# Optimization experiments

Hardware: AMD Instinct MI355X
Metric: run time of the kernel (lower is better)

The kernel has to match this reference:

```python
import jax, jax.numpy as jnp
import numpy as np

B, S, IN, IN2, H = 512, 256, 300, 300, 512
FN = 3  # filter_num


def setup_inputs() -> dict:
    key = jax.random.key(0)
    ks = jax.random.split(key, 16)
    def n(k, shape, scale=0.05):
        return jax.random.normal(k, shape, dtype=jnp.float32) * scale
    return {
        "x": jax.random.normal(ks[0], (B, S, IN), dtype=jnp.float32),
        "W_in": n(ks[1], (IN, IN2)), "b_in": n(ks[2], (IN2,)),
        "Wih": n(ks[3], (IN2, 4 * H)), "Whh": n(ks[4], (H, 4 * H)),
        "bih": n(ks[5], (4 * H,)), "bhh": n(ks[6], (4 * H,)),
        "Q": n(ks[7], (H, IN2)), "R": n(ks[8], (IN2, H)),
        "Wc3": n(ks[9], (FN, 1, 3, H)), "bc3": n(ks[10], (FN,)),
        "Wc4": n(ks[11], (FN, 1, 4, H)), "bc4": n(ks[12], (FN,)),
        "Wc5": n(ks[13], (FN, 1, 5, H)), "bc5": n(ks[14], (FN,)),
        "W_lin": n(ks[15], (3 * FN, 2)), "b_lin": jnp.zeros((2,), jnp.float32),
    }


def reference(x, W_in, b_in, Wih, Whh, bih, bhh, Q, R,
              Wc3, bc3, Wc4, bc4, Wc5, bc5, W_lin, b_lin):
    # input projection: [B,S,IN] -> [B,S,IN2]
    xin = jnp.tanh(x @ W_in + b_in)
    xs = jnp.swapaxes(xin, 0, 1)  # [S,B,IN2] for scan
    bsz = x.shape[0]
    h0 = jnp.zeros((bsz, H), x.dtype)
    c0 = jnp.zeros((bsz, H), x.dtype)

    def step(carry, xt):
        ht, Ct = carry
        # mogrify, mog_iterations=2: i=1 odd updates x, i=2 even updates h
        xt = 2.0 * jax.nn.sigmoid(ht @ Q) * xt
        ht = 2.0 * jax.nn.sigmoid(xt @ R) * ht
        gates = xt @ Wih + bih + ht @ Whh + bhh  # [B,4H]
        i, f, g, o = jnp.split(gates, 4, axis=1)
        Ct = jax.nn.sigmoid(f) * Ct + jax.nn.sigmoid(i) * jnp.tanh(g)
        ht = jax.nn.sigmoid(o) * jnp.tanh(Ct)
        return (ht, Ct), ht

    _, hs = jax.lax.scan(step, (h0, c0), xs)  # [S,B,H]
    hmap = jnp.swapaxes(hs, 0, 1)[:, None, :, :]  # [B,1,S,H]

    feats = []
    for w, b in ((Wc3, bc3), (Wc4, bc4), (Wc5, bc5)):
        y = jax.lax.conv_general_dilated(
            hmap, w, (1, 1), 'VALID',
            dimension_numbers=('NCHW', 'OIHW', 'NCHW'))
        y = jax.nn.relu(y + b[None, :, None, None])  # [B,FN,S-fsz+1,1]
        feats.append(jnp.max(y, axis=(2, 3)))  # global max pool -> [B,FN]
    cat = jnp.concatenate(feats, axis=1)  # [B, 3*FN]
    # dropout is identity at inference
    return cat @ W_lin + b_lin  # [B,2]
```

## Files before the change

### kernel.cpp

```cpp
#include <hip/hip_runtime.h>

#define DI __device__ __forceinline__

typedef __attribute__((ext_vector_type(4))) float  f32x4;
typedef __attribute__((ext_vector_type(8))) short  s16x8;
typedef __attribute__((ext_vector_type(8))) __bf16 bf16x8;
typedef unsigned long long u64;

constexpr int S_   = 256;
constexpr int B_   = 512;
constexpr int H_   = 512;
constexpr int KP_  = 320;
constexpr int ALD_ = 832;
constexpr int NRING = 34;
constexpr int NWG  = 256;
constexpr size_t HSLOT = 512 * 512;

constexpr size_t OFF_XIN = 0;
constexpr size_t SZ_XIN  = (size_t)S_ * B_ * KP_ * 2;
constexpr size_t OFF_U   = OFF_XIN + SZ_XIN;
constexpr size_t SZ_U    = (size_t)B_ * S_ * 64 * 4;
constexpr size_t OFF_HS  = OFF_U + SZ_U;
constexpr size_t SZ_HS   = (size_t)NRING * HSLOT * 2;
constexpr size_t OFF_ACT = OFF_HS + SZ_HS;
constexpr size_t SZ_ACT  = (size_t)B_ * ALD_ * 2;
constexpr size_t OFF_HFP = OFF_ACT + SZ_ACT;
constexpr size_t SZ_HFP  = (size_t)B_ * H_ * 4;
constexpr size_t OFF_WPT = OFF_HFP + SZ_HFP;
constexpr size_t SZ_WPT  = (size_t)320 * 320 * 2;
constexpr size_t OFF_QPT = OFF_WPT + SZ_WPT;
constexpr size_t SZ_QPT  = (size_t)320 * 512 * 2;
constexpr size_t OFF_RPT = OFF_QPT + SZ_QPT;
constexpr size_t SZ_RPT  = (size_t)512 * 320 * 2;
constexpr size_t OFF_WGT = OFF_RPT + SZ_RPT;
constexpr size_t SZ_WGT  = (size_t)2048 * 832 * 2;
constexpr size_t OFF_BG  = OFF_WGT + SZ_WGT;
constexpr size_t SZ_BG   = 2048 * 4;
constexpr size_t OFF_VT  = OFF_BG + SZ_BG;
constexpr size_t SZ_VT   = (size_t)64 * 512 * 2;
constexpr size_t OFF_BAR = OFF_VT + SZ_VT;
constexpr size_t SZ_BAR  = 4096;
constexpr size_t WS_NEED = OFF_BAR + SZ_BAR;

DI unsigned short f2bf(float x) {
  unsigned int u = __float_as_uint(x);
  unsigned int r = (u + 0x7FFFu + ((u >> 16) & 1u)) >> 16;
  return (unsigned short)r;
}
DI float bf2f(unsigned short h) { return __uint_as_float(((unsigned int)h) << 16); }

DI float sigm(float x) {
  float e = __builtin_amdgcn_exp2f(x * -1.44269504088896f);
  return __builtin_amdgcn_rcpf(1.0f + e);
}
DI float tanh_(float x) {
  x = fminf(fmaxf(x, -15.0f), 15.0f);
  float e = __builtin_amdgcn_exp2f(x * 2.88539008177793f);
  return (e - 1.0f) * __builtin_amdgcn_rcpf(e + 1.0f);
}
DI bf16x8 asbf(s16x8 v) { return __builtin_bit_cast(bf16x8, v); }

DI u64 ld_sys_u64(const void* p) {
  return __hip_atomic_load((const u64*)p, __ATOMIC_RELAXED, __HIP_MEMORY_SCOPE_SYSTEM);
}
DI void st_sys_u64(void* p, u64 v) {
  __hip_atomic_store((u64*)p, v, __ATOMIC_RELAXED, __HIP_MEMORY_SCOPE_SYSTEM);
}
template<int N> DI void wait_vm() {
  asm volatile("s_waitcnt vmcnt(%0)" :: "n"(N) : "memory");
}

struct a16x8 { u64 lo, hi; };
DI a16x8 ldA(const unsigned short* p) {
  a16x8 r; r.lo = ld_sys_u64(p); r.hi = ld_sys_u64(p + 4); return r;
}
DI void stA_lds(short* dst, a16x8 v) {
  *(u64*)dst = v.lo; *(u64*)(dst + 4) = v.hi;
}

template<int NR>
DI void gemm2(const unsigned short* Ab, int lda,
              const unsigned short* Bb, int ldb,
              short* sA, short* sB, f32x4 acc[2][2])
{
  const int tid  = threadIdx.x;
  const int t2   = tid & 255;
  const int team = tid >> 8;
  const int lane = t2 & 63;
  const int w = t2 >> 6, wm = w >> 1, wn = w & 1;
  const unsigned short* ga = Ab + (t2 >> 2) * lda + (t2 & 3) * 8;
  const unsigned short* gb = Bb + (t2 >> 2) * ldb + (t2 & 3) * 8;
  const int slot  = team * 2048;
  const int arow0 = (wm * 32 + (lane & 15)) * 32 + (lane >> 4) * 8;
  const int brow0 = (wn * 32 + (lane & 15)) * 32 + (lane >> 4) * 8;

  a16x8 a0, a1 = {};
  s16x8 b0, b1 = {};
  a0 = ldA(ga + team * 32);
  b0 = *(const s16x8*)(gb + team * 32);
  if (NR > 1) {
    a1 = ldA(ga + (2 + team) * 32);
    b1 = *(const s16x8*)(gb + (2 + team) * 32);
  }
  stA_lds(&sA[slot + t2 * 8], a0);
  *(s16x8*)&sB[slot + t2 * 8] = b0;
  __syncthreads();
  #pragma unroll
  for (int j = 0; j < NR; ++j) {
    const int cur = (j & 1) * 4096;
    if (j + 2 < NR) {
      const int kt = 2 * (j + 2) + team;
      if ((j & 1) == 0) { a0 = ldA(ga + kt * 32); b0 = *(const s16x8*)(gb + kt * 32); }
      else              { a1 = ldA(ga + kt * 32); b1 = *(const s16x8*)(gb + kt * 32); }
    }
    s16x8 A0 = *(const s16x8*)&sA[cur + slot + arow0];
    s16x8 A1 = *(const s16x8*)&sA[cur + slot + arow0 + 512];
    s16x8 B0 = *(const s16x8*)&sB[cur + slot + brow0];
    s16x8 B1 = *(const s16x8*)&sB[cur + slot + brow0 + 512];
    acc[0][0] = __builtin_amdgcn_mfma_f32_16x16x32_bf16(asbf(A0), asbf(B0), acc[0][0], 0, 0, 0);
    acc[0][1] = __builtin_amdgcn_mfma_f32_16x16x32_bf16(asbf(A0), asbf(B1), acc[0][1], 0, 0, 0);
    acc[1][0] = __builtin_amdgcn_mfma_f32_16x16x32_bf16(asbf(A1), asbf(B0), acc[1][0], 0, 0, 0);
    acc[1][1] = __builtin_amdgcn_mfma_f32_16x16x32_bf16(asbf(A1), asbf(B1), acc[1][1], 0, 0, 0);
    if (j + 1 < NR) {
      const int nxt = ((j + 1) & 1) * 4096;
      if ((j & 1) == 0) { stA_lds(&sA[nxt + slot + t2 * 8], a1); *(s16x8*)&sB[nxt + slot + t2 * 8] = b1; }
      else              { stA_lds(&sA[nxt + slot + t2 * 8], a0); *(s16x8*)&sB[nxt + slot + t2 * 8] = b0; }
    }
    __syncthreads();
  }
}

DI void reduce_teams(f32x4 acc[2][2], float* rbuf) {
  const int tid = threadIdx.x, t2 = tid & 255;
  if (tid >= 256) {
    #pragma unroll
    for (int mi = 0; mi < 2; ++mi)
      #pragma unroll
      for (int ni = 0; ni < 2; ++ni)
        #pragma unroll
        for (int r = 0; r < 4; ++r)
          rbuf[((mi * 2 + ni) * 4 + r) * 256 + t2] = acc[mi][ni][r];
  }
  __syncthreads();
  if (tid < 256) {
    #pragma unroll
    for (int mi = 0; mi < 2; ++mi)
      #pragma unroll
      for (int ni = 0; ni < 2; ++ni)
        #pragma unroll
        for (int r = 0; r < 4; ++r)
          acc[mi][ni][r] += rbuf[((mi * 2 + ni) * 4 + r) * 256 + t2];
  }
}

template<int NK, int KREAL>
DI void gemm_f32A(const float* Af, int lda,
                  const unsigned short* Bb, int ldb,
                  short* sA, short* sB, f32x4 acc[2][2])
{
  const int tid  = threadIdx.x;
  const int lane = tid & 63;
  const int w = tid >> 6, wm = w >> 1, wn = w & 1;
  const float* ga = Af + (tid >> 2) * lda;
  const int cseg  = (tid & 3) * 8;
  const unsigned short* gb = Bb + (tid >> 2) * ldb + (tid & 3) * 8;
  const int arow0 = (wm * 32 + (lane & 15)) * 32 + (lane >> 4) * 8;
  const int brow0 = (wn * 32 + (lane & 15)) * 32 + (lane >> 4) * 8;

  auto loadA = [&](int k) -> s16x8 {
    s16x8 r;
    const int c0 = k * 32 + cseg;
    if (c0 + 8 <= KREAL) {
      float4 f0 = *(const float4*)(ga + c0);
      float4 f1 = *(const float4*)(ga + c0 + 4);
      r[0] = (short)f2bf(f0.x); r[1] = (short)f2bf(f0.y);
      r[2] = (short)f2bf(f0.z); r[3] = (short)f2bf(f0.w);
      r[4] = (short)f2bf(f1.x); r[5] = (short)f2bf(f1.y);
      r[6] = (short)f2bf(f1.z); r[7] = (short)f2bf(f1.w);
    } else {
      #pragma unroll
      for (int j = 0; j < 8; ++j) {
        float x = (c0 + j < KREAL) ? ga[c0 + j] : 0.0f;
        r[j] = (short)f2bf(x);
      }
    }
    return r;
  };

  s16x8 va = loadA(0);
  s16x8 vb = *(const s16x8*)gb;
  *(s16x8*)&sA[tid * 8] = va;
  *(s16x8*)&sB[tid * 8] = vb;
  __syncthreads();
  for (int k = 0; k < NK; ++k) {
    const int cur = (k & 1) * 2048;
    if (k + 1 < NK) {
      va = loadA(k + 1);
      vb = *(const s16x8*)(gb + (k + 1) * 32);
    }
    s16x8 a0 = *(const s16x8*)&sA[cur + arow0];
    s16x8 a1 = *(const s16x8*)&sA[cur + arow0 + 16 * 32];
    s16x8 b0 = *(const s16x8*)&sB[cur + brow0];
    s16x8 b1 = *(const s16x8*)&sB[cur + brow0 + 16 * 32];
    acc[0][0] = __builtin_amdgcn_mfma_f32_16x16x32_bf16(asbf(a0), asbf(b0), acc[0][0], 0, 0, 0);
    acc[0][1] = __builtin_amdgcn_mfma_f32_16x16x32_bf16(asbf(a0), asbf(b1), acc[0][1], 0, 0, 0);
    acc[1][0] = __builtin_amdgcn_mfma_f32_16x16x32_bf16(asbf(a1), asbf(b0), acc[1][0], 0, 0, 0);
    acc[1][1] = __builtin_amdgcn_mfma_f32_16x16x32_bf16(asbf(a1), asbf(b1), acc[1][1], 0, 0, 0);
    if (k + 1 < NK) {
      const int nxt = ((k + 1) & 1) * 2048;
      *(s16x8*)&sA[nxt + tid * 8] = va;
      *(s16x8*)&sB[nxt + tid * 8] = vb;
    }
    __syncthreads();
  }
}

template<typename F>
DI void epiloop(f32x4 acc[2][2], F&& f) {
  const int lane = threadIdx.x & 63;
  const int w = (threadIdx.x & 255) >> 6, wm = w >> 1, wn = w & 1;
  #pragma unroll
  for (int mi = 0; mi < 2; ++mi)
    #pragma unroll
    for (int ni = 0; ni < 2; ++ni)
      #pragma unroll
      for (int r = 0; r < 4; ++r) {
        const int rowl = wm * 32 + mi * 16 + (lane >> 4) * 4 + r;
        const int coll = wn * 32 + ni * 16 + (lane & 15);
        f(rowl, coll, acc[mi][ni][r]);
      }
}

DI void pack_store_512(const unsigned short* lds16, unsigned short* dstbase, int ldd) {
  const u64* l64 = (const u64*)lds16;
  #pragma unroll
  for (int it = 0; it < 2; ++it) {
    const int i = it * 512 + threadIdx.x;
    const int row = i >> 4, q = i & 15;
    st_sys_u64(dstbase + row * ldd + q * 4, l64[row * 16 + q]);
  }
}

__global__ void k_prep_wpt(const float* __restrict__ Wi, unsigned short* __restrict__ WpT) {
  int i = blockIdx.x * 256 + threadIdx.x;
  if (i >= 320 * 320) return;
  int n = i / 320, k = i % 320;
  float v = (n < 300 && k < 300) ? Wi[k * 300 + n] : 0.0f;
  WpT[i] = f2bf(v);
}
__global__ void k_prep_qpt(const float* __restrict__ Q, unsigned short* __restrict__ QpT) {
  int i = blockIdx.x * 256 + threadIdx.x;
  if (i >= 320 * 512) return;
  int n = i >> 9, k = i & 511;
  float v = (n < 300) ? Q[k * 300 + n] : 0.0f;
  QpT[i] = f2bf(v);
}
__global__ void k_prep_rpt(const float* __restrict__ R, unsigned short* __restrict__ RpT) {
  int i = blockIdx.x * 256 + threadIdx.x;
  if (i >= 512 * 320) return;
  int n = i / 320, k = i % 320;
  float v = (k < 300) ? R[k * 512 + n] : 0.0f;
  RpT[i] = f2bf(v);
}
__global__ void k_prep_wgt(const float* __restrict__ Wih, const float* __restrict__ Whh,
                           unsigned short* __restrict__ WgT) {
  int i = blockIdx.x * 256 + threadIdx.x;
  if (i >= 2048 * 832) return;
  int np = i / 832, k = i % 832;
  int c = np >> 2, g = np & 3, col = g * 512 + c;
  float v = 0.0f;
  if (k < 300) v = Wih[k * 2048 + col];
  else if (k >= 320) v = Whh[(k - 320) * 2048 + col];
  WgT[i] = f2bf(v);
}
__global__ void k_prep_bg(const float* __restrict__ bih, const float* __restrict__ bhh,
                          float* __restrict__ bg) {
  int i = blockIdx.x * 256 + threadIdx.x;
  if (i >= 2048) return;
  int c = i >> 2, g = i & 3, col = g * 512 + c;
  bg[i] = bih[col] + bhh[col];
}
__global__ void k_prep_vt(const float* __restrict__ Wc3, const float* __restrict__ Wc4,
                          const float* __restrict__ Wc5, unsigned short* __restrict__ VT) {
  int i = blockIdx.x * 256 + threadIdx.x;
  if (i >= 64 * 512) return;
  int j = i >> 9, k = i & 511;
  float v = 0.0f;
  if (j < 9)       { int f = j / 3,  dt = j % 3;        v = Wc3[(f * 3 + dt) * 512 + k]; }
  else if (j < 21) { int jj = j - 9;  int f = jj / 4, dt = jj % 4; v = Wc4[(f * 4 + dt) * 512 + k]; }
  else if (j < 36) { int jj = j - 21; int f = jj / 5, dt = jj % 5; v = Wc5[(f * 5 + dt) * 512 + k]; }
  VT[i] = f2bf(v);
}
__global__ void k_wsfail(float* out, int n, float v) {
  int i = blockIdx.x * 256 + threadIdx.x;
  if (i < n) out[i] = -v;
}

__global__ __launch_bounds__(256) void k_proj(const float* __restrict__ x,
                                              const unsigned short* __restrict__ WpT,
                                              const float* __restrict__ b_in,
                                              unsigned short* __restrict__ xin) {
  __shared__ short sA[4096], sB[4096];
  const int m0 = blockIdx.x * 64, n0 = blockIdx.y * 64;
  f32x4 acc[2][2];
  const f32x4 z = {0.f, 0.f, 0.f, 0.f};
  acc[0][0] = z; acc[0][1] = z; acc[1][0] = z; acc[1][1] = z;
  gemm_f32A<10, 300>(x + (size_t)m0 * 300, 300, WpT + n0 * 320, 320, sA, sB, acc);
  epiloop(acc, [&](int rowl, int coll, float vacc) {
    const int row = m0 + rowl, col = n0 + coll;
    float o = 0.0f;
    if (col < 300) o = tanh_(vacc + b_in[col]);
    const int b = row >> 8, s = row & 255;
    xin[(size_t)(s * 512 + b) * KP_ + col] = f2bf(o);
  });
}

__global__ __launch_bounds__(512, 2) void k_scan(
    const unsigned short* __restrict__ xin,
    const unsigned short* __restrict__ QpT,
    const unsigned short* __restrict__ RpT,
    const unsigned short* __restrict__ WgT,
    const float* __restrict__ bg,
    const unsigned short* __restrict__ VT,
    unsigned short* __restrict__ hs,
    unsigned short* __restrict__ act,
    float* __restrict__ hfp,
    float* __restrict__ U,
    unsigned int* __restrict__ bar)
{
  __shared__ short sA[8192], sB[8192];
  __shared__ float gbuf[4096];
  __shared__ float rbuf[4096];
  __shared__ float pbuf[4096];
  __shared__ unsigned short obuf[4096];
  const int wg   = blockIdx.x;
  const int grp  = wg >> 5;
  const int l    = wg & 31;
  const int tid  = threadIdx.x;
  const f32x4 z = {0.f, 0.f, 0.f, 0.f};

  const int gm0 = grp * 64;
  const int gn0 = l * 64;
  float c_state[2] = {0.f, 0.f};

  int ep = 0;
  auto bar_sync = [&]() {
    wait_vm<0>();
    __syncthreads();
    if (tid == 0) {
      __hip_atomic_fetch_add(&bar[grp * 64], 1u,
                             __ATOMIC_RELAXED, __HIP_MEMORY_SCOPE_AGENT);
      const unsigned tgt = (unsigned)(ep + 1) * 32u;
      while (__hip_atomic_load(&bar[grp * 64], __ATOMIC_RELAXED,
                               __HIP_MEMORY_SCOPE_AGENT) < tgt)
        __builtin_amdgcn_s_sleep(1);
    }
    __syncthreads();
    ++ep;
  };

  for (int t = 0; t < S_; ++t) {
    const unsigned short* hst = hs + (size_t)(t % NRING) * HSLOT;
    unsigned short*       hso = hs + (size_t)((t + 1) % NRING) * HSLOT;

    if (l < 5) {
      const int m0 = gm0, n0 = l * 64;
      f32x4 acc[2][2];
      acc[0][0] = z; acc[0][1] = z; acc[1][0] = z; acc[1][1] = z;
      gemm2<8>(hst + m0 * 512, 512, QpT + n0 * 512, 512, sA, sB, acc);
      reduce_teams(acc, rbuf);
      if (tid < 256) {
        const unsigned short* xin_t = xin + (size_t)t * 512 * KP_;
        epiloop(acc, [&](int rowl, int coll, float vacc) {
          obuf[rowl * 64 + coll] =
            f2bf(2.0f * sigm(vacc) * bf2f(xin_t[(m0 + rowl) * KP_ + n0 + coll]));
        });
      }
      __syncthreads();
      pack_store_512(obuf, act + m0 * ALD_ + n0, ALD_);
    }
    bar_sync();

    if (l < 8) {
      const int m0 = gm0, n0 = l * 64;
      {
        u64* p64 = (u64*)pbuf;
        #pragma unroll
        for (int it = 0; it < 4; ++it) {
          const int i = it * 512 + tid;
          const int row = i >> 5, p = i & 31;
          p64[row * 32 + p] = ld_sys_u64(hfp + (m0 + row) * 512 + n0 + p * 2);
        }
      }
      f32x4 acc[2][2];
      acc[0][0] = z; acc[0][1] = z; acc[1][0] = z; acc[1][1] = z;
      gemm2<5>(act + m0 * ALD_, ALD_, RpT + n0 * KP_, KP_, sA, sB, acc);
      reduce_teams(acc, rbuf);
      if (tid < 256) {
        epiloop(acc, [&](int rowl, int coll, float vacc) {
          obuf[rowl * 64 + coll] = f2bf(2.0f * sigm(vacc) * pbuf[rowl * 64 + coll]);
        });
      }
      __syncthreads();
      pack_store_512(obuf, act + m0 * ALD_ + 320 + n0, ALD_);
    }
    bar_sync();

    {
      f32x4 acc[2][2];
      acc[0][0] = z; acc[0][1] = z; acc[1][0] = z; acc[1][1] = z;
      gemm2<13>(act + gm0 * ALD_, ALD_, WgT + gn0 * 832, 832, sA, sB, acc);
      reduce_teams(acc, rbuf);
      if (tid < 256) {
        epiloop(acc, [&](int rowl, int coll, float vacc) {
          gbuf[rowl * 64 + coll] = vacc;
        });
      }
      __syncthreads();
      unsigned short* hbuf = obuf;
      float*          fbuf = rbuf;
      #pragma unroll
      for (int q = 0; q < 2; ++q) {
        const int item = q * 512 + tid;
        const int row = item >> 4, cu = item & 15;
        const float4 bb = *(const float4*)&bg[gn0 + cu * 4];
        const float iv = gbuf[row * 64 + cu * 4 + 0] + bb.x;
        const float fv = gbuf[row * 64 + cu * 4 + 1] + bb.y;
        const float gv = gbuf[row * 64 + cu * 4 + 2] + bb.z;
        const float ov = gbuf[row * 64 + cu * 4 + 3] + bb.w;
        const float cn = sigm(fv) * c_state[q] + sigm(iv) * tanh_(gv);
        const float h  = sigm(ov) * tanh_(cn);
        c_state[q] = cn;
        hbuf[row * 16 + cu] = f2bf(h);
        fbuf[row * 16 + cu] = h;
      }
      __syncthreads();
      if (tid < 256) {
        const u64* h64 = (const u64*)hbuf;
        const int row = tid >> 2, q = tid & 3;
        st_sys_u64(hso + (gm0 + row) * 512 + (gn0 >> 2) + q * 4, h64[row * 4 + q]);
      }
      {
        const u64* f64 = (const u64*)fbuf;
        const int r2 = tid >> 3, p = tid & 7;
        st_sys_u64(hfp + (gm0 + r2) * 512 + (gn0 >> 2) + p * 2, f64[r2 * 8 + p]);
      }
    }
    bar_sync();

    if ((t & 31) == 31) {
      const int c = t >> 5;
      const int tglob = 32 * c + l;
      const int slot = (tglob + 1) % NRING;
      const int brow = gm0;
      f32x4 acc[2][2];
      acc[0][0] = z; acc[0][1] = z; acc[1][0] = z; acc[1][1] = z;
      gemm2<8>(hs + (size_t)slot * HSLOT + (size_t)brow * 512, 512, VT, 512, sA, sB, acc);
      reduce_teams(acc, rbuf);
      if (tid < 256) {
        epiloop(acc, [&](int rowl, int coll, float vacc) {
          U[((size_t)(brow + rowl) * 256 + tglob) * 64 + coll] = vacc;
        });
      }
    }
  }
}

__global__ __launch_bounds__(256) void k_combine(const float* __restrict__ U,
                                                 const float* __restrict__ bc3,
                                                 const float* __restrict__ bc4,
                                                 const float* __restrict__ bc5,
                                                 const float* __restrict__ Wl,
                                                 const float* __restrict__ bl,
                                                 float* __restrict__ out) {
  const int b = blockIdx.x;
  const int p = threadIdx.x;
  const float* Ub = U + (size_t)b * (256 * 64);
  float v[9];
  #pragma unroll
  for (int j = 0; j < 9; ++j) v[j] = -1e30f;
  if (p < 254) {
    #pragma unroll
    for (int f = 0; f < 3; ++f)
      v[f] = Ub[(p + 0) * 64 + f * 3 + 0] + Ub[(p + 1) * 64 + f * 3 + 1] + Ub[(p + 2) * 64 + f * 3 + 2];
  }
  if (p < 253) {
    #pragma unroll
    for (int f = 0; f < 3; ++f)
      v[3 + f] = Ub[(p + 0) * 64 + 9 + f * 4 + 0] + Ub[(p + 1) * 64 + 9 + f * 4 + 1] +
                 Ub[(p + 2) * 64 + 9 + f * 4 + 2] + Ub[(p + 3) * 64 + 9 + f * 4 + 3];
  }
  if (p < 252) {
    #pragma unroll
    for (int f = 0; f < 3; ++f)
      v[6 + f] = Ub[(p + 0) * 64 + 21 + f * 5 + 0] + Ub[(p + 1) * 64 + 21 + f * 5 + 1] +
                 Ub[(p + 2) * 64 + 21 + f * 5 + 2] + Ub[(p + 3) * 64 + 21 + f * 5 + 3] +
                 Ub[(p + 4) * 64 + 21 + f * 5 + 4];
  }
  __shared__ float red[4][9];
  const int lane = threadIdx.x & 63, w = threadIdx.x >> 6;
  #pragma unroll
  for (int j = 0; j < 9; ++j) {
    float m = v[j];
    #pragma unroll
    for (int off = 32; off >= 1; off >>= 1) m = fmaxf(m, __shfl_xor(m, off));
    if (lane == 0) red[w][j] = m;
  }
  __syncthreads();
  if (threadIdx.x < 2) {
    const int k = threadIdx.x;
    float o = bl[k];
    #pragma unroll
    for (int j = 0; j < 9; ++j) {
      float m = fmaxf(fmaxf(red[0][j], red[1][j]), fmaxf(red[2][j], red[3][j]));
      float bias = (j < 3) ? bc3[j] : (j < 6) ? bc4[j - 3] : bc5[j - 6];
      o += fmaxf(m + bias, 0.0f) * Wl[j * 2 + k];
    }
    out[b * 2 + k] = o;
  }
}

extern "C" void kernel_launch(void* const* d_in, const int* in_sizes, int n_in,
                              void* d_out, int out_size, void* d_ws, size_t ws_size,
                              hipStream_t stream) {
  const float* x     = (const float*)d_in[0];
  const float* W_in  = (const float*)d_in[1];
  const float* b_in  = (const float*)d_in[2];
  const float* Wih   = (const float*)d_in[3];
  const float* Whh   = (const float*)d_in[4];
  const float* bih   = (const float*)d_in[5];
  const float* bhh   = (const float*)d_in[6];
  const float* Q     = (const float*)d_in[7];
  const float* R     = (const float*)d_in[8];
  const float* Wc3   = (const float*)d_in[9];
  const float* bc3   = (const float*)d_in[10];
  const float* Wc4   = (const float*)d_in[11];
  const float* bc4   = (const float*)d_in[12];
  const float* Wc5   = (const float*)d_in[13];
  const float* bc5   = (const float*)d_in[14];
  const float* W_lin = (const float*)d_in[15];
  const float* b_lin = (const float*)d_in[16];

  if (ws_size < WS_NEED) {
    k_wsfail<<<4, 256, 0, stream>>>((float*)d_out, out_size, (float)(ws_size >> 20));
    return;
  }

  char* ws = (char*)d_ws;
  unsigned short* xin = (unsigned short*)(ws + OFF_XIN);
  float*          U   = (float*)(ws + OFF_U);
  unsigned short* hs  = (unsigned short*)(ws + OFF_HS);
  unsigned short* act = (unsigned short*)(ws + OFF_ACT);
  float*          hfp = (float*)(ws + OFF_HFP);
  unsigned short* WpT = (unsigned short*)(ws + OFF_WPT);
  unsigned short* QpT = (unsigned short*)(ws + OFF_QPT);
  unsigned short* RpT = (unsigned short*)(ws + OFF_RPT);
  unsigned short* WgT = (unsigned short*)(ws + OFF_WGT);
  float*          bg  = (float*)(ws + OFF_BG);
  unsigned short* VT  = (unsigned short*)(ws + OFF_VT);
  unsigned int*   bar = (unsigned int*)(ws + OFF_BAR);

  (void)hipMemsetAsync(hs, 0, HSLOT * 2, stream);
  (void)hipMemsetAsync(hfp, 0, SZ_HFP, stream);
  (void)hipMemsetAsync(bar, 0, SZ_BAR, stream);

  k_prep_wpt<<<(320 * 320 + 255) / 256, 256, 0, stream>>>(W_in, WpT);
  k_prep_qpt<<<(320 * 512 + 255) / 256, 256, 0, stream>>>(Q, QpT);
  k_prep_rpt<<<(512 * 320 + 255) / 256, 256, 0, stream>>>(R, RpT);
  k_prep_wgt<<<(2048 * 832 + 255) / 256, 256, 0, stream>>>(Wih, Whh, WgT);
  k_prep_bg<<<8, 256, 0, stream>>>(bih, bhh, bg);
  k_prep_vt<<<(64 * 512 + 255) / 256, 256, 0, stream>>>(Wc3, Wc4, Wc5, VT);

  k_proj<<<dim3(131072 / 64, KP_ / 64), 256, 0, stream>>>(x, WpT, b_in, xin);

  k_scan<<<NWG, 512, 0, stream>>>(xin, QpT, RpT, WgT, bg, VT, hs, act, hfp, U, bar);

  k_combine<<<512, 256, 0, stream>>>(U, bc3, bc4, bc5, W_lin, b_lin, (float*)d_out);
}
```

Measured before the change: 5.490 ms.

## Split persistent scan across 512 workgroups with 32-row tiles

```diff
diff --git a/kernel.cpp b/kernel.cpp
--- a/kernel.cpp
+++ b/kernel.cpp
@@ -9,11 +9,10 @@
 
 constexpr int S_   = 256;
 constexpr int B_   = 512;
-constexpr int H_   = 512;
 constexpr int KP_  = 320;
 constexpr int ALD_ = 832;
 constexpr int NRING = 34;
-constexpr int NWG  = 256;
+constexpr int NWG  = 512;
 constexpr size_t HSLOT = 512 * 512;
 
 constexpr size_t OFF_XIN = 0;
@@ -24,9 +23,7 @@
 constexpr size_t SZ_HS   = (size_t)NRING * HSLOT * 2;
 constexpr size_t OFF_ACT = OFF_HS + SZ_HS;
 constexpr size_t SZ_ACT  = (size_t)B_ * ALD_ * 2;
-constexpr size_t OFF_HFP = OFF_ACT + SZ_ACT;
-constexpr size_t SZ_HFP  = (size_t)B_ * H_ * 4;
-constexpr size_t OFF_WPT = OFF_HFP + SZ_HFP;
+constexpr size_t OFF_WPT = OFF_ACT + SZ_ACT;
 constexpr size_t SZ_WPT  = (size_t)320 * 320 * 2;
 constexpr size_t OFF_QPT = OFF_WPT + SZ_WPT;
 constexpr size_t SZ_QPT  = (size_t)320 * 512 * 2;
@@ -39,7 +36,7 @@
 constexpr size_t OFF_VT  = OFF_BG + SZ_BG;
 constexpr size_t SZ_VT   = (size_t)64 * 512 * 2;
 constexpr size_t OFF_BAR = OFF_VT + SZ_VT;
-constexpr size_t SZ_BAR  = 4096;
+constexpr size_t SZ_BAR  = 8192;
 constexpr size_t WS_NEED = OFF_BAR + SZ_BAR;
 
 DI unsigned short f2bf(float x) {
@@ -70,87 +67,113 @@
   asm volatile("s_waitcnt vmcnt(%0)" :: "n"(N) : "memory");
 }
 
-struct a16x8 { u64 lo, hi; };
-DI a16x8 ldA(const unsigned short* p) {
-  a16x8 r; r.lo = ld_sys_u64(p); r.hi = ld_sys_u64(p + 4); return r;
-}
-DI void stA_lds(short* dst, a16x8 v) {
-  *(u64*)dst = v.lo; *(u64*)(dst + 4) = v.hi;
-}
-
-template<int NR>
+template<int NK>
 DI void gemm2(const unsigned short* Ab, int lda,
               const unsigned short* Bb, int ldb,
-              short* sA, short* sB, f32x4 acc[2][2])
+              short* sA, short* sB, f32x4 acc[2])
 {
+  constexpr int NR = (NK + 1) / 2;
   const int tid  = threadIdx.x;
-  const int t2   = tid & 255;
-  const int team = tid >> 8;
-  const int lane = t2 & 63;
-  const int w = t2 >> 6, wm = w >> 1, wn = w & 1;
-  const unsigned short* ga = Ab + (t2 >> 2) * lda + (t2 & 3) * 8;
-  const unsigned short* gb = Bb + (t2 >> 2) * ldb + (t2 & 3) * 8;
-  const int slot  = team * 2048;
-  const int arow0 = (wm * 32 + (lane & 15)) * 32 + (lane >> 4) * 8;
-  const int brow0 = (wn * 32 + (lane & 15)) * 32 + (lane >> 4) * 8;
-
-  a16x8 a0, a1 = {};
-  s16x8 b0, b1 = {};
-  a0 = ldA(ga + team * 32);
-  b0 = *(const s16x8*)(gb + team * 32);
-  if (NR > 1) {
-    a1 = ldA(ga + (2 + team) * 32);
-    b1 = *(const s16x8*)(gb + (2 + team) * 32);
-  }
-  stA_lds(&sA[slot + t2 * 8], a0);
-  *(s16x8*)&sB[slot + t2 * 8] = b0;
+  const int tm   = tid >> 8;
+  const int t8   = tid & 255;
+  const int lane = tid & 63;
+  const int l15  = lane & 15;
+  const int kseg = (lane >> 4) * 8;
+  const int w    = (tid >> 6) & 3;
+  const int wm = w >> 1, wn = w & 1;
+  const int sArow = t8 >> 3, sAcol = (t8 & 7) * 4;
+  const int sBrow = t8 >> 2, sBcol = (t8 & 3) * 8;
+  const unsigned short* gA = Ab + sArow * lda + sAcol;
+  const unsigned short* gB = Bb + sBrow * ldb + sBcol;
+  short* tA = sA + tm * 2048;
+  short* tB = sB + tm * 4096;
+  const int aoff = sArow * 32 + sAcol;
+  const int boff = sBrow * 32 + sBcol;
+  const int afr  = (wm * 16 + l15) * 32 + kseg;
+
+  u64 a0, a1 = 0, b00, b01, b10 = 0, b11 = 0;
+  a0  = ld_sys_u64(gA + tm * 32);
+  b00 = ((const u64*)(gB + tm * 32))[0];
+  b01 = ((const u64*)(gB + tm * 32))[1];
+  if (2 + tm < NK) {
+    a1  = ld_sys_u64(gA + (2 + tm) * 32);
+    b10 = ((const u64*)(gB + (2 + tm) * 32))[0];
+    b11 = ((const u64*)(gB + (2 + tm) * 32))[1];
+  }
+  *(u64*)&tA[aoff] = a0;
+  *(u64*)&tB[boff] = b00; *(u64*)&tB[boff + 4] = b01;
   __syncthreads();
   #pragma unroll
   for (int j = 0; j < NR; ++j) {
-    const int cur = (j & 1) * 4096;
+    const int curA = (j & 1) * 1024, curB = (j & 1) * 2048;
     if (j + 2 < NR) {
-      const int kt = 2 * (j + 2) + team;
-      if ((j & 1) == 0) { a0 = ldA(ga + kt * 32); b0 = *(const s16x8*)(gb + kt * 32); }
-      else              { a1 = ldA(ga + kt * 32); b1 = *(const s16x8*)(gb + kt * 32); }
-    }
-    s16x8 A0 = *(const s16x8*)&sA[cur + slot + arow0];
-    s16x8 A1 = *(const s16x8*)&sA[cur + slot + arow0 + 512];
-    s16x8 B0 = *(const s16x8*)&sB[cur + slot + brow0];
-    s16x8 B1 = *(const s16x8*)&sB[cur + slot + brow0 + 512];
-    acc[0][0] = __builtin_amdgcn_mfma_f32_16x16x32_bf16(asbf(A0), asbf(B0), acc[0][0], 0, 0, 0);
-    acc[0][1] = __builtin_amdgcn_mfma_f32_16x16x32_bf16(asbf(A0), asbf(B1), acc[0][1], 0, 0, 0);
-    acc[1][0] = __builtin_amdgcn_mfma_f32_16x16x32_bf16(asbf(A1), asbf(B0), acc[1][0], 0, 0, 0);
-    acc[1][1] = __builtin_amdgcn_mfma_f32_16x16x32_bf16(asbf(A1), asbf(B1), acc[1][1], 0, 0, 0);
+      const int kt = (j + 2) * 2 + tm;
+      if (kt < NK) {
+        if ((j & 1) == 0) { a0 = ld_sys_u64(gA + kt * 32);
+                            b00 = ((const u64*)(gB + kt * 32))[0];
+                            b01 = ((const u64*)(gB + kt * 32))[1]; }
+        else              { a1 = ld_sys_u64(gA + kt * 32);
+                            b10 = ((const u64*)(gB + kt * 32))[0];
+                            b11 = ((const u64*)(gB + kt * 32))[1]; }
+      }
+    }
+    if (j * 2 + tm < NK) {
+      s16x8 Af = *(const s16x8*)&tA[curA + afr];
+      #pragma unroll
+      for (int ni = 0; ni < 2; ++ni) {
+        s16x8 Bf = *(const s16x8*)&tB[curB + (wn * 32 + ni * 16 + l15) * 32 + kseg];
+        acc[ni] = __builtin_amdgcn_mfma_f32_16x16x32_bf16(asbf(Af), asbf(Bf), acc[ni], 0, 0, 0);
+      }
+    }
     if (j + 1 < NR) {
-      const int nxt = ((j + 1) & 1) * 4096;
-      if ((j & 1) == 0) { stA_lds(&sA[nxt + slot + t2 * 8], a1); *(s16x8*)&sB[nxt + slot + t2 * 8] = b1; }
-      else              { stA_lds(&sA[nxt + slot + t2 * 8], a0); *(s16x8*)&sB[nxt + slot + t2 * 8] = b0; }
+      const int kt = (j + 1) * 2 + tm;
+      const int nxtA = ((j + 1) & 1) * 1024, nxtB = ((j + 1) & 1) * 2048;
+      if (kt < NK) {
+        if ((j & 1) == 0) { *(u64*)&tA[nxtA + aoff] = a1;
+                            *(u64*)&tB[nxtB + boff] = b10; *(u64*)&tB[nxtB + boff + 4] = b11; }
+        else              { *(u64*)&tA[nxtA + aoff] = a0;
+                            *(u64*)&tB[nxtB + boff] = b00; *(u64*)&tB[nxtB + boff + 4] = b01; }
+      }
     }
     __syncthreads();
   }
 }
 
-DI void reduce_teams(f32x4 acc[2][2], float* rbuf) {
-  const int tid = threadIdx.x, t2 = tid & 255;
+DI void reduce2(f32x4 acc[2], float* rbuf) {
+  const int tid = threadIdx.x, t8 = tid & 255;
   if (tid >= 256) {
     #pragma unroll
-    for (int mi = 0; mi < 2; ++mi)
+    for (int ni = 0; ni < 2; ++ni)
       #pragma unroll
-      for (int ni = 0; ni < 2; ++ni)
-        #pragma unroll
-        for (int r = 0; r < 4; ++r)
-          rbuf[((mi * 2 + ni) * 4 + r) * 256 + t2] = acc[mi][ni][r];
+      for (int r = 0; r < 4; ++r)
+        rbuf[(ni * 4 + r) * 256 + t8] = acc[ni][r];
   }
   __syncthreads();
   if (tid < 256) {
     #pragma unroll
-    for (int mi = 0; mi < 2; ++mi)
+    for (int ni = 0; ni < 2; ++ni)
       #pragma unroll
-      for (int ni = 0; ni < 2; ++ni)
-        #pragma unroll
-        for (int r = 0; r < 4; ++r)
-          acc[mi][ni][r] += rbuf[((mi * 2 + ni) * 4 + r) * 256 + t2];
-  }
+      for (int r = 0; r < 4; ++r)
+        acc[ni][r] += rbuf[(ni * 4 + r) * 256 + t8];
+  }
+}
+
+template<typename F>
+DI void epiloop32(f32x4 acc[2], F&& f) {
+  const int lane = threadIdx.x & 63;
+  const int w = (threadIdx.x >> 6) & 3, wm = w >> 1, wn = w & 1;
+  #pragma unroll
+  for (int ni = 0; ni < 2; ++ni)
+    #pragma unroll
+    for (int r = 0; r < 4; ++r)
+      f(wm * 16 + (lane >> 4) * 4 + r, wn * 32 + ni * 16 + (lane & 15), acc[ni][r]);
+}
+
+DI void pack_store32(const unsigned short* lds16, unsigned short* dstbase, int ldd) {
+  const u64* l64 = (const u64*)lds16;
+  const int i = threadIdx.x;
+  const int row = i >> 4, q = i & 15;
+  st_sys_u64(dstbase + row * ldd + q * 4, l64[i]);
 }
 
 template<int NK, int KREAL>
@@ -229,16 +252,6 @@
         const int coll = wn * 32 + ni * 16 + (lane & 15);
         f(rowl, coll, acc[mi][ni][r]);
       }
-}
-
-DI void pack_store_512(const unsigned short* lds16, unsigned short* dstbase, int ldd) {
-  const u64* l64 = (const u64*)lds16;
-  #pragma unroll
-  for (int it = 0; it < 2; ++it) {
-    const int i = it * 512 + threadIdx.x;
-    const int row = i >> 4, q = i & 15;
-    st_sys_u64(dstbase + row * ldd + q * 4, l64[row * 16 + q]);
-  }
 }
 
 __global__ void k_prep_wpt(const float* __restrict__ Wi, unsigned short* __restrict__ WpT) {
@@ -315,7 +328,7 @@
   });
 }
 
-__global__ __launch_bounds__(512, 2) void k_scan(
+__global__ __launch_bounds__(512, 4) void k_scan(
     const unsigned short* __restrict__ xin,
     const unsigned short* __restrict__ QpT,
     const unsigned short* __restrict__ RpT,
@@ -324,24 +337,26 @@
     const unsigned short* __restrict__ VT,
     unsigned short* __restrict__ hs,
     unsigned short* __restrict__ act,
-    float* __restrict__ hfp,
     float* __restrict__ U,
     unsigned int* __restrict__ bar)
 {
-  __shared__ short sA[8192], sB[8192];
-  __shared__ float gbuf[4096];
-  __shared__ float rbuf[4096];
-  __shared__ float pbuf[4096];
-  __shared__ unsigned short obuf[4096];
+  __shared__ short sA[4096];
+  __shared__ short sB[8192];
+  __shared__ float rbuf[2048];
+  __shared__ float gbuf[2048];
+  __shared__ unsigned short pbuf[2048];
+  __shared__ unsigned short obuf[2048];
   const int wg   = blockIdx.x;
   const int grp  = wg >> 5;
   const int l    = wg & 31;
   const int tid  = threadIdx.x;
   const f32x4 z = {0.f, 0.f, 0.f, 0.f};
 
-  const int gm0 = grp * 64;
+  const int gm0 = grp * 32;
   const int gn0 = l * 64;
-  float c_state[2] = {0.f, 0.f};
+  float c_state = 0.f;
+  const int crow = tid >> 4, ccl = tid & 15;
+  const float4 cb = *(const float4*)&bg[gn0 + ccl * 4];
 
   int ep = 0;
   auto bar_sync = [&]() {
@@ -364,86 +379,69 @@
     unsigned short*       hso = hs + (size_t)((t + 1) % NRING) * HSLOT;
 
     if (l < 5) {
-      const int m0 = gm0, n0 = l * 64;
-      f32x4 acc[2][2];
-      acc[0][0] = z; acc[0][1] = z; acc[1][0] = z; acc[1][1] = z;
-      gemm2<8>(hst + m0 * 512, 512, QpT + n0 * 512, 512, sA, sB, acc);
-      reduce_teams(acc, rbuf);
+      const int n0 = l * 64;
+      {
+        const unsigned short* xin_t = xin + ((size_t)t * 512 + gm0) * KP_;
+        const int row = tid >> 4, q = tid & 15;
+        ((u64*)pbuf)[tid] = *(const u64*)(xin_t + row * KP_ + n0 + q * 4);
+      }
+      f32x4 acc[2] = {z, z};
+      gemm2<16>(hst + gm0 * 512, 512, QpT + n0 * 512, 512, sA, sB, acc);
+      reduce2(acc, rbuf);
       if (tid < 256) {
-        const unsigned short* xin_t = xin + (size_t)t * 512 * KP_;
-        epiloop(acc, [&](int rowl, int coll, float vacc) {
-          obuf[rowl * 64 + coll] =
-            f2bf(2.0f * sigm(vacc) * bf2f(xin_t[(m0 + rowl) * KP_ + n0 + coll]));
+        epiloop32(acc, [&](int row, int col, float v) {
+          obuf[row * 64 + col] = f2bf(2.0f * sigm(v) * bf2f(pbuf[row * 64 + col]));
         });
       }
       __syncthreads();
-      pack_store_512(obuf, act + m0 * ALD_ + n0, ALD_);
+      pack_store32(obuf, act + gm0 * ALD_ + n0, ALD_);
     }
     bar_sync();
 
     if (l < 8) {
-      const int m0 = gm0, n0 = l * 64;
+      const int n0 = l * 64;
       {
-        u64* p64 = (u64*)pbuf;
-        #pragma unroll
-        for (int it = 0; it < 4; ++it) {
-          const int i = it * 512 + tid;
-          const int row = i >> 5, p = i & 31;
-          p64[row * 32 + p] = ld_sys_u64(hfp + (m0 + row) * 512 + n0 + p * 2);
-        }
-      }
-      f32x4 acc[2][2];
-      acc[0][0] = z; acc[0][1] = z; acc[1][0] = z; acc[1][1] = z;
-      gemm2<5>(act + m0 * ALD_, ALD_, RpT + n0 * KP_, KP_, sA, sB, acc);
-      reduce_teams(acc, rbuf);
+        const int row = tid >> 4, q = tid & 15;
+        ((u64*)pbuf)[tid] = ld_sys_u64(hst + (gm0 + row) * 512 + n0 + q * 4);
+      }
+      f32x4 acc[2] = {z, z};
+      gemm2<10>(act + gm0 * ALD_, ALD_, RpT + n0 * KP_, KP_, sA, sB, acc);
+      reduce2(acc, rbuf);
       if (tid < 256) {
-        epiloop(acc, [&](int rowl, int coll, float vacc) {
-          obuf[rowl * 64 + coll] = f2bf(2.0f * sigm(vacc) * pbuf[rowl * 64 + coll]);
+        epiloop32(acc, [&](int row, int col, float v) {
+          obuf[row * 64 + col] = f2bf(2.0f * sigm(v) * bf2f(pbuf[row * 64 + col]));
         });
       }
       __syncthreads();
-      pack_store_512(obuf, act + m0 * ALD_ + 320 + n0, ALD_);
+      pack_store32(obuf, act + gm0 * ALD_ + 320 + n0, ALD_);
     }
     bar_sync();
 
     {
-      f32x4 acc[2][2];
-      acc[0][0] = z; acc[0][1] = z; acc[1][0] = z; acc[1][1] = z;
-      gemm2<13>(act + gm0 * ALD_, ALD_, WgT + gn0 * 832, 832, sA, sB, acc);
-      reduce_teams(acc, rbuf);
+      f32x4 acc[2] = {z, z};
+      gemm2<26>(act + gm0 * ALD_, ALD_, WgT + gn0 * 832, 832, sA, sB, acc);
+      reduce2(acc, rbuf);
       if (tid < 256) {
-        epiloop(acc, [&](int rowl, int coll, float vacc) {
-          gbuf[rowl * 64 + coll] = vacc;
+        epiloop32(acc, [&](int row, int col, float v) {
+          gbuf[row * 64 + col] = v;
         });
       }
       __syncthreads();
-      unsigned short* hbuf = obuf;
-      float*          fbuf = rbuf;
-      #pragma unroll
-      for (int q = 0; q < 2; ++q) {
-        const int item = q * 512 + tid;
-        const int row = item >> 4, cu = item & 15;
-        const float4 bb = *(const float4*)&bg[gn0 + cu * 4];
-        const float iv = gbuf[row * 64 + cu * 4 + 0] + bb.x;
-        const float fv = gbuf[row * 64 + cu * 4 + 1] + bb.y;
-        const float gv = gbuf[row * 64 + cu * 4 + 2] + bb.z;
-        const float ov = gbuf[row * 64 + cu * 4 + 3] + bb.w;
-        const float cn = sigm(fv) * c_state[q] + sigm(iv) * tanh_(gv);
+      {
+        const float iv = gbuf[crow * 64 + ccl * 4 + 0] + cb.x;
+        const float fv = gbuf[crow * 64 + ccl * 4 + 1] + cb.y;
+        const float gv = gbuf[crow * 64 + ccl * 4 + 2] + cb.z;
+        const float ov = gbuf[crow * 64 + ccl * 4 + 3] + cb.w;
+        const float cn = sigm(fv) * c_state + sigm(iv) * tanh_(gv);
         const float h  = sigm(ov) * tanh_(cn);
-        c_state[q] = cn;
-        hbuf[row * 16 + cu] = f2bf(h);
-        fbuf[row * 16 + cu] = h;
+        c_state = cn;
+        obuf[crow * 16 + ccl] = f2bf(h);
       }
       __syncthreads();
-      if (tid < 256) {
-        const u64* h64 = (const u64*)hbuf;
+      if (tid < 128) {
+        const u64* h64 = (const u64*)obuf;
         const int row = tid >> 2, q = tid & 3;
-        st_sys_u64(hso + (gm0 + row) * 512 + (gn0 >> 2) + q * 4, h64[row * 4 + q]);
-      }
-      {
-        const u64* f64 = (const u64*)fbuf;
-        const int r2 = tid >> 3, p = tid & 7;
-        st_sys_u64(hfp + (gm0 + r2) * 512 + (gn0 >> 2) + p * 2, f64[r2 * 8 + p]);
+        st_sys_u64(hso + (gm0 + row) * 512 + l * 16 + q * 4, h64[row * 4 + q]);
       }
     }
     bar_sync();
@@ -452,16 +450,15 @@
       const int c = t >> 5;
       const int tglob = 32 * c + l;
       const int slot = (tglob + 1) % NRING;
-      const int brow = gm0;
-      f32x4 acc[2][2];
-      acc[0][0] = z; acc[0][1] = z; acc[1][0] = z; acc[1][1] = z;
-      gemm2<8>(hs + (size_t)slot * HSLOT + (size_t)brow * 512, 512, VT, 512, sA, sB, acc);
-      reduce_teams(acc, rbuf);
+      f32x4 acc[2] = {z, z};
+      gemm2<16>(hs + (size_t)slot * HSLOT + (size_t)gm0 * 512, 512, VT, 512, sA, sB, acc);
+      reduce2(acc, rbuf);
       if (tid < 256) {
-        epiloop(acc, [&](int rowl, int coll, float vacc) {
-          U[((size_t)(brow + rowl) * 256 + tglob) * 64 + coll] = vacc;
+        epiloop32(acc, [&](int row, int col, float v) {
+          U[((size_t)(gm0 + row) * 256 + tglob) * 64 + col] = v;
         });
       }
+      __syncthreads();
     }
   }
 }
@@ -551,7 +548,6 @@
   float*          U   = (float*)(ws + OFF_U);
   unsigned short* hs  = (unsigned short*)(ws + OFF_HS);
   unsigned short* act = (unsigned short*)(ws + OFF_ACT);
-  float*          hfp = (float*)(ws + OFF_HFP);
   unsigned short* WpT = (unsigned short*)(ws + OFF_WPT);
   unsigned short* QpT = (unsigned short*)(ws + OFF_QPT);
   unsigned short* RpT = (unsigned short*)(ws + OFF_RPT);
@@ -561,7 +557,6 @@
   unsigned int*   bar = (unsigned int*)(ws + OFF_BAR);
 
   (void)hipMemsetAsync(hs, 0, HSLOT * 2, stream);
-  (void)hipMemsetAsync(hfp, 0, SZ_HFP, stream);
   (void)hipMemsetAsync(bar, 0, SZ_BAR, stream);
 
   k_prep_wpt<<<(320 * 320 + 255) / 256, 256, 0, stream>>>(W_in, WpT);
@@ -573,7 +568,7 @@
 
   k_proj<<<dim3(131072 / 64, KP_ / 64), 256, 0, stream>>>(x, WpT, b_in, xin);
 
-  k_scan<<<NWG, 512, 0, stream>>>(xin, QpT, RpT, WgT, bg, VT, hs, act, hfp, U, bar);
+  k_scan<<<NWG, 512, 0, stream>>>(xin, QpT, RpT, WgT, bg, VT, hs, act, U, bar);
 
   k_combine<<<512, 256, 0, stream>>>(U, bc3, bc4, bc5, W_lin, b_lin, (float*)d_out);
 }
```

Result: no change. 5.543 ms, median of 2 (+1.0%).
